# Performance work log

Measured on AMD Instinct MI355X. Metric: run time of the kernel, lower is better.

The kernel has to match this reference:

```python
import jax, jax.numpy as jnp
import numpy as np

TOP_K = 2
N_EXPERTS = 8

def setup_inputs() -> dict:
    key = jax.random.key(0)
    k1, k2, k3, k4 = jax.random.split(key, 4)
    B, C, L, O, E = 8, 4096, 1024, 1024, N_EXPERTS
    scale = 1.0 / np.sqrt(L)
    return {
        "x": jax.random.normal(k1, (B, C, L), dtype=jnp.float32),
        "gate_w": jax.random.normal(k2, (E, L), dtype=jnp.float32) * scale,
        "expert_w": jax.random.normal(k3, (E, O, L), dtype=jnp.float32) * scale,
        "expert_b": jax.random.normal(k4, (E, O), dtype=jnp.float32) * scale,
    }

def reference(x, gate_w, expert_w, expert_b):
    B, C, L = x.shape
    E, O, _ = expert_w.shape
    xt = x.reshape(-1, L)                                  # [T, L], T = B*C
    router_logits = jnp.einsum('tl,el->te', xt, gate_w)    # [T, E]
    probs = jax.nn.softmax(router_logits.astype(jnp.float32), axis=-1)
    routing_weights, selected = jax.lax.top_k(probs, TOP_K)  # [T, K] each
    # combine weight per (token, expert): sum of top-k weights routed to that expert
    comb = jnp.sum(jax.nn.one_hot(selected, E, dtype=routing_weights.dtype)
                   * routing_weights[..., None], axis=1)   # [T, E]
    comb = comb.astype(x.dtype)
    out = jnp.zeros((xt.shape[0], O), dtype=x.dtype)
    for e in range(E):  # small fixed expert loop; masked dense combine
        ye = xt @ expert_w[e].T + expert_b[e]              # [T, O]
        out = out + ye * comb[:, e:e + 1]
    return out.reshape(B, C, O)
```

## Files before the change

### kernel.cpp

```cpp
#include <hip/hip_runtime.h>
#include <cstdint>
#include <cstddef>

#define E_EXP 8
#define LDIM 1024
#define ODIM 1024
#define NPAIR 64

#define BM 256
#define BN 128
#define BK 32
#define NKT (LDIM / BK)
#define MAXRT 160
#define GEMM_GRID (MAXRT * 8)
#define CPX (GEMM_GRID / 8)

typedef __bf16 bf16x8 __attribute__((ext_vector_type(8)));
typedef float f32x4 __attribute__((ext_vector_type(4)));

__device__ __forceinline__ unsigned short f2bf(float f) {
  uint32_t u = __float_as_uint(f);
  u += 0x7FFFu + ((u >> 16) & 1u);
  return (unsigned short)(u >> 16);
}

__device__ __forceinline__ void gload_lds16(const void* g, void* l) {
  __builtin_amdgcn_global_load_lds(
      (const __attribute__((address_space(1))) unsigned int*)g,
      (__attribute__((address_space(3))) unsigned int*)l, 16, 0, 0);
}

__global__ __launch_bounds__(256) void route_kernel(
    const float* __restrict__ x, const float* __restrict__ gate,
    unsigned short* __restrict__ xb, int* __restrict__ sel,
    float2* __restrict__ pw, int T)
{
  const int wid = threadIdx.x >> 6, lane = threadIdx.x & 63;
  const int tok = blockIdx.x * 4 + wid;
  if (tok >= T) return;
  const float* xr = x + (size_t)tok * LDIM;
  unsigned short* xbr = xb + (size_t)tok * LDIM;

  float acc[E_EXP];
#pragma unroll
  for (int e = 0; e < E_EXP; ++e) acc[e] = 0.f;

#pragma unroll
  for (int it = 0; it < 4; ++it) {
    const int c = it * 256 + lane * 4;
    float4 xv = *(const float4*)(xr + c);
    ushort4 bvv;
    bvv.x = f2bf(xv.x); bvv.y = f2bf(xv.y); bvv.z = f2bf(xv.z); bvv.w = f2bf(xv.w);
    *(ushort4*)(xbr + c) = bvv;
#pragma unroll
    for (int e = 0; e < E_EXP; ++e) {
      float4 gv = *(const float4*)(gate + e * LDIM + c);
      acc[e] += xv.x * gv.x + xv.y * gv.y + xv.z * gv.z + xv.w * gv.w;
    }
  }
#pragma unroll
  for (int off = 32; off >= 1; off >>= 1) {
#pragma unroll
    for (int e = 0; e < E_EXP; ++e) acc[e] += __shfl_xor(acc[e], off, 64);
  }
  if (lane == 0) {
    int i1 = 0; float m1 = acc[0];
#pragma unroll
    for (int e = 1; e < E_EXP; ++e) if (acc[e] > m1) { m1 = acc[e]; i1 = e; }
    int i2 = -1; float m2 = -1e30f;
#pragma unroll
    for (int e = 0; e < E_EXP; ++e) if (e != i1 && acc[e] > m2) { m2 = acc[e]; i2 = e; }
    float s = 0.f;
#pragma unroll
    for (int e = 0; e < E_EXP; ++e) s += __expf(acc[e] - m1);
    const float inv = 1.f / s;
    sel[tok] = i1 | (i2 << 4);
    pw[tok] = make_float2(inv, __expf(m2 - m1) * inv);
  }
}

__global__ __launch_bounds__(256) void hist_kernel(
    const int* __restrict__ sel, int* __restrict__ hist2d, int T)
{
  __shared__ int h[NPAIR];
  const int tid = threadIdx.x;
  if (tid < NPAIR) h[tid] = 0;
  __syncthreads();
  const int t0 = blockIdx.x * 2048;
#pragma unroll
  for (int i = 0; i < 8; ++i) {
    const int t = t0 + i * 256 + tid;
    if (t < T) {
      const int s = sel[t];
      const int i1 = s & 15, i2 = (s >> 4) & 15;
      const int lo = i1 < i2 ? i1 : i2, hi = i1 < i2 ? i2 : i1;
      atomicAdd(&h[lo * 8 + hi], 1);
    }
  }
  __syncthreads();
  if (tid < NPAIR) hist2d[blockIdx.x * NPAIR + tid] = h[tid];
}

__global__ void finalize_kernel(
    const int* __restrict__ hist2d, int nb,
    int* __restrict__ blockBase, int4* __restrict__ desc, int* __restrict__ meta)
{
  __shared__ int pcnt[NPAIR], pbase[NPAIR];
  const int p = threadIdx.x;
  if (p < NPAIR) {
    int c = 0;
#pragma unroll 4
    for (int b = 0; b < nb; ++b) c += hist2d[b * NPAIR + p];
    pcnt[p] = c;
  }
  __syncthreads();
  if (p == 0) {
    int s = 0;
    for (int q = 0; q < NPAIR; ++q) { pbase[q] = s; s += pcnt[q]; }
  }
  __syncthreads();
  if (p < NPAIR) {
    int run = pbase[p];
    for (int b = 0; b < nb; ++b) {
      blockBase[b * NPAIR + p] = run;
      run += hist2d[b * NPAIR + p];
    }
  }
  if (p == 0) {
    int rt = 0;
    for (int q = 0; q < NPAIR; ++q) {
      const int lo = q >> 3, hi = q & 7;
      for (int j = 0; j * BM < pcnt[q]; ++j) {
        int rows = pcnt[q] - j * BM; if (rows > BM) rows = BM;
        desc[rt] = make_int4(lo | (hi << 8), pbase[q] + j * BM, rows, 0);
        ++rt;
      }
    }
    meta[0] = rt;
  }
}

__global__ __launch_bounds__(256) void scatter_kernel(
    const int* __restrict__ sel, const float2* __restrict__ pw,
    const int* __restrict__ blockBase, int* __restrict__ tokC,
    float2* __restrict__ wC, int T)
{
  __shared__ int cur[NPAIR];
  const int tid = threadIdx.x;
  if (tid < NPAIR) cur[tid] = blockBase[blockIdx.x * NPAIR + tid];
  __syncthreads();
  const int t0 = blockIdx.x * 2048;
#pragma unroll
  for (int i = 0; i < 8; ++i) {
    const int t = t0 + i * 256 + tid;
    if (t < T) {
      const int s = sel[t];
      const int i1 = s & 15, i2 = (s >> 4) & 15;
      const float2 w = pw[t];
      const int lo = i1 < i2 ? i1 : i2, hi = i1 < i2 ? i2 : i1;
      const float wlo = i1 < i2 ? w.x : w.y;
      const float whi = i1 < i2 ? w.y : w.x;
      const int pos = atomicAdd(&cur[lo * 8 + hi], 1);
      tokC[pos] = t;
      wC[pos] = make_float2(wlo, whi);
    }
  }
}

__global__ __launch_bounds__(256) void convw_kernel(
    const float* __restrict__ w, unsigned short* __restrict__ wb, int n4)
{
  int i = blockIdx.x * 256 + threadIdx.x;
  if (i >= n4) return;
  float4 v = *(const float4*)(w + (size_t)i * 4);
  ushort4 b;
  b.x = f2bf(v.x); b.y = f2bf(v.y); b.z = f2bf(v.z); b.w = f2bf(v.w);
  *(ushort4*)(wb + (size_t)i * 4) = b;
}

__global__ __launch_bounds__(512, 2) void moe_gemm_pair(
    const unsigned short* __restrict__ xb, const unsigned short* __restrict__ wb,
    const float* __restrict__ bias, const int4* __restrict__ desc,
    const int* __restrict__ meta, const int* __restrict__ tokC,
    const float2* __restrict__ wC, float* __restrict__ out)
{
  __shared__ __align__(16) unsigned short ldsA[3][BM * BK];
  __shared__ __align__(16) unsigned short ldsB[3][2 * BN * BK];
  const int tid = threadIdx.x;
  const int lane = tid & 63, w = tid >> 6;
  const int wm = w >> 2, wn = w & 3;

  const int totalRT = meta[0];
  const int swz = ((int)blockIdx.x & 7) * CPX + ((int)blockIdx.x >> 3);
  if (swz >= totalRT * 8) return;
  const int rt = swz >> 3, colTile = swz & 7;
  const int4 d = desc[rt];
  const int lo = d.x & 255, hi = d.x >> 8;
  const int start = d.y, ce = d.z;
  const int* tokL = tokC + start;
  const float2* wgtL = wC + start;

  const int s = lane & 3;
  const int rA0 = w * 32 + (lane >> 2);
  const int rA1 = rA0 + 16;
  const int gA0 = s ^ ((rA0 >> 1) & 3);
  const int gA1 = s ^ ((rA1 >> 1) & 3);
  const int tA0 = tokL[rA0 < ce ? rA0 : ce - 1];
  const int tA1 = tokL[rA1 < ce ? rA1 : ce - 1];
  const char* aSrc0 = (const char*)(xb + (size_t)tA0 * LDIM) + gA0 * 16;
  const char* aSrc1 = (const char*)(xb + (size_t)tA1 * LDIM) + gA1 * 16;
  const int rB = w * 16 + (lane >> 2);
  const int gB = s ^ ((rB >> 1) & 3);
  const int colB = colTile * BN + rB;
  const char* bSrcLo = (const char*)(wb + ((size_t)lo * ODIM + colB) * LDIM) + gB * 16;
  const char* bSrcHi = (const char*)(wb + ((size_t)hi * ODIM + colB) * LDIM) + gB * 16;

  int offA[8], offB[2];
#pragma unroll
  for (int fr = 0; fr < 8; ++fr) {
    const int r = wm * 128 + fr * 16 + (lane & 15);
    offA[fr] = r * BK + (((lane >> 4) ^ ((r >> 1) & 3)) * 8);
  }
#pragma unroll
  for (int fc = 0; fc < 2; ++fc) {
    const int r = wn * 32 + fc * 16 + (lane & 15);
    offB[fc] = r * BK + (((lane >> 4) ^ ((r >> 1) & 3)) * 8);
  }

  auto stage = [&](int b, int kt) {
    const int kb = kt * 64;
    gload_lds16(aSrc0 + kb, &ldsA[b][w * 1024]);
    gload_lds16(aSrc1 + kb, &ldsA[b][w * 1024 + 512]);
    gload_lds16(bSrcLo + kb, &ldsB[b][w * 512]);
    gload_lds16(bSrcHi + kb, &ldsB[b][4096 + w * 512]);
  };

  f32x4 acc[2][8][2] = {};

  stage(0, 0); stage(1, 1);
  asm volatile("s_waitcnt vmcnt(4)" ::: "memory");
  __builtin_amdgcn_s_barrier();

  int buf = 0;
#pragma unroll 1
  for (int kt = 0; kt < NKT; ++kt) {
    const unsigned short* As = &ldsA[buf][0];
    const unsigned short* Bs = &ldsB[buf][0];
    bf16x8 af[8], bl0, bl1, bh0, bh1;
#pragma unroll
    for (int fr = 0; fr < 8; ++fr) af[fr] = *(const bf16x8*)(As + offA[fr]);
    bl0 = *(const bf16x8*)(Bs + offB[0]);
    bl1 = *(const bf16x8*)(Bs + offB[1]);
    bh0 = *(const bf16x8*)(Bs + 4096 + offB[0]);
    bh1 = *(const bf16x8*)(Bs + 4096 + offB[1]);

    int sb = buf + 2; if (sb > 2) sb -= 3;
    stage(sb, kt + 2 < NKT ? kt + 2 : NKT - 1);

    __builtin_amdgcn_s_setprio(1);
#pragma unroll
    for (int fr = 0; fr < 8; ++fr) {
      acc[0][fr][0] = __builtin_amdgcn_mfma_f32_16x16x32_bf16(af[fr], bl0, acc[0][fr][0], 0, 0, 0);
      acc[0][fr][1] = __builtin_amdgcn_mfma_f32_16x16x32_bf16(af[fr], bl1, acc[0][fr][1], 0, 0, 0);
      acc[1][fr][0] = __builtin_amdgcn_mfma_f32_16x16x32_bf16(af[fr], bh0, acc[1][fr][0], 0, 0, 0);
      acc[1][fr][1] = __builtin_amdgcn_mfma_f32_16x16x32_bf16(af[fr], bh1, acc[1][fr][1], 0, 0, 0);
    }
    __builtin_amdgcn_s_setprio(0);

    asm volatile("s_waitcnt lgkmcnt(0)" ::: "memory");
    asm volatile("s_waitcnt vmcnt(4)" ::: "memory");
    __builtin_amdgcn_s_barrier();
    buf = (buf == 2) ? 0 : buf + 1;
  }

  int cols[2]; float bLo[2], bHi[2];
#pragma unroll
  for (int fc = 0; fc < 2; ++fc) {
    cols[fc] = colTile * BN + wn * 32 + fc * 16 + (lane & 15);
    bLo[fc] = bias[lo * ODIM + cols[fc]];
    bHi[fc] = bias[hi * ODIM + cols[fc]];
  }
#pragma unroll
  for (int fr = 0; fr < 8; ++fr) {
#pragma unroll
    for (int rr = 0; rr < 4; ++rr) {
      const int row = wm * 128 + fr * 16 + (lane >> 4) * 4 + rr;
      if (row < ce) {
        const int tok = tokL[row];
        const float2 ww = wgtL[row];
        float* orow = out + (size_t)tok * ODIM;
#pragma unroll
        for (int fc = 0; fc < 2; ++fc)
          orow[cols[fc]] = ww.x * (acc[0][fr][fc][rr] + bLo[fc]) +
                           ww.y * (acc[1][fr][fc][rr] + bHi[fc]);
      }
    }
  }
}

__global__ __launch_bounds__(256) void naive_moe(
    const float* __restrict__ x, const float* __restrict__ gate,
    const float* __restrict__ ew, const float* __restrict__ eb,
    float* __restrict__ out, int T)
{
  const int tok = blockIdx.x, tid = threadIdx.x;
  __shared__ float xs[LDIM];
  __shared__ float logits[E_EXP];
  __shared__ float sw1, sw2; __shared__ int si1, si2;
  for (int i = tid; i < LDIM; i += 256) xs[i] = x[(size_t)tok * LDIM + i];
  __syncthreads();
  const int wid = tid >> 6, lane = tid & 63;
  for (int e = wid; e < E_EXP; e += 4) {
    float a = 0.f;
    for (int i = lane; i < LDIM; i += 64) a += xs[i] * gate[e * LDIM + i];
    for (int off = 32; off >= 1; off >>= 1) a += __shfl_xor(a, off, 64);
    if (lane == 0) logits[e] = a;
  }
  __syncthreads();
  if (tid == 0) {
    int i1 = 0; float m1 = logits[0];
    for (int e = 1; e < E_EXP; ++e) if (logits[e] > m1) { m1 = logits[e]; i1 = e; }
    int i2 = -1; float m2 = -1e30f;
    for (int e = 0; e < E_EXP; ++e) if (e != i1 && logits[e] > m2) { m2 = logits[e]; i2 = e; }
    float s = 0.f;
    for (int e = 0; e < E_EXP; ++e) s += __expf(logits[e] - m1);
    si1 = i1; si2 = i2; sw1 = 1.f / s; sw2 = __expf(m2 - m1) / s;
  }
  __syncthreads();
  const int i1 = si1, i2 = si2; const float w1 = sw1, w2 = sw2;
  for (int o = tid; o < ODIM; o += 256) {
    float a1 = 0.f, a2 = 0.f;
    const float* p1 = ew + ((size_t)i1 * ODIM + o) * LDIM;
    const float* p2 = ew + ((size_t)i2 * ODIM + o) * LDIM;
    for (int l = 0; l < LDIM; ++l) { a1 += xs[l] * p1[l]; a2 += xs[l] * p2[l]; }
    out[(size_t)tok * ODIM + o] =
        w1 * (a1 + eb[i1 * ODIM + o]) + w2 * (a2 + eb[i2 * ODIM + o]);
  }
}

extern "C" void kernel_launch(void* const* d_in, const int* in_sizes, int n_in,
                              void* d_out, int out_size, void* d_ws, size_t ws_size,
                              hipStream_t stream) {
  const float* x    = (const float*)d_in[0];
  const float* gate = (const float*)d_in[1];
  const float* ew   = (const float*)d_in[2];
  const float* eb   = (const float*)d_in[3];
  float* out = (float*)d_out;
  const int T = in_sizes[0] / LDIM;
  const int NB = (T + 2047) / 2048;

  const size_t offSel   = 0;
  const size_t offPw    = offSel + (size_t)T * 4;
  const size_t offHist  = offPw + (size_t)T * 8;
  const size_t offBBase = offHist + (size_t)NB * NPAIR * 4;
  const size_t offDesc  = offBBase + (size_t)NB * NPAIR * 4;
  const size_t offMeta  = offDesc + (size_t)MAXRT * 16;
  const size_t offTokC  = offMeta + 256;
  const size_t offWC    = offTokC + (size_t)T * 4;
  const size_t offXb    = offWC + (size_t)T * 8;
  const size_t offWb    = offXb + (size_t)T * LDIM * 2;
  const size_t need     = offWb + (size_t)E_EXP * ODIM * LDIM * 2;

  if (ws_size < need) {
    naive_moe<<<T, 256, 0, stream>>>(x, gate, ew, eb, out, T);
    return;
  }

  char* ws = (char*)d_ws;

  route_kernel<<<(T + 3) / 4, 256, 0, stream>>>(
      x, gate, (unsigned short*)(ws + offXb), (int*)(ws + offSel),
      (float2*)(ws + offPw), T);

  const int n4 = E_EXP * ODIM * LDIM / 4;
  convw_kernel<<<(n4 + 255) / 256, 256, 0, stream>>>(ew, (unsigned short*)(ws + offWb), n4);

  hist_kernel<<<NB, 256, 0, stream>>>(
      (const int*)(ws + offSel), (int*)(ws + offHist), T);

  finalize_kernel<<<1, 64, 0, stream>>>(
      (const int*)(ws + offHist), NB, (int*)(ws + offBBase),
      (int4*)(ws + offDesc), (int*)(ws + offMeta));

  scatter_kernel<<<NB, 256, 0, stream>>>(
      (const int*)(ws + offSel), (const float2*)(ws + offPw),
      (const int*)(ws + offBBase), (int*)(ws + offTokC),
      (float2*)(ws + offWC), T);

  moe_gemm_pair<<<GEMM_GRID, 512, 0, stream>>>(
      (const unsigned short*)(ws + offXb), (const unsigned short*)(ws + offWb),
      eb, (const int4*)(ws + offDesc), (const int*)(ws + offMeta),
      (const int*)(ws + offTokC), (const float2*)(ws + offWC), out);
}
```

Measured before the change: 273.7 us.

## Switch expert GEMM to 32x32x16 MFMA and batch four tokens per routing wave

The grouped expert GEMM now uses 32x32x16 bf16 MFMA tiles in place of 16x16x32. This halves the MFMA instruction count and changes the LDS fragment offsets and the epilogue row mapping to match. Separately, each routing wave now handles four tokens, so every gate-weight load is reused across four tokens and the grid is a quarter the size. The risks are a higher register count for the 16-wide accumulators, and the routing shuffle reduction now covering four times as many values.

```diff
diff --git a/kernel.cpp b/kernel.cpp
--- a/kernel.cpp
+++ b/kernel.cpp
@@ -17,6 +17,7 @@
 
 typedef __bf16 bf16x8 __attribute__((ext_vector_type(8)));
 typedef float f32x4 __attribute__((ext_vector_type(4)));
+typedef float f32x16 __attribute__((ext_vector_type(16)));
 
 __device__ __forceinline__ unsigned short f2bf(float f) {
   uint32_t u = __float_as_uint(f);
@@ -36,46 +37,63 @@
     float2* __restrict__ pw, int T)
 {
   const int wid = threadIdx.x >> 6, lane = threadIdx.x & 63;
-  const int tok = blockIdx.x * 4 + wid;
-  if (tok >= T) return;
-  const float* xr = x + (size_t)tok * LDIM;
-  unsigned short* xbr = xb + (size_t)tok * LDIM;
-
-  float acc[E_EXP];
-#pragma unroll
-  for (int e = 0; e < E_EXP; ++e) acc[e] = 0.f;
+  const int tokBase = blockIdx.x * 16 + wid * 4;
+  if (tokBase >= T) return;
+  const float* xr = x + (size_t)tokBase * LDIM;
+  unsigned short* xbr = xb + (size_t)tokBase * LDIM;
+
+  float acc[4][E_EXP];
+#pragma unroll
+  for (int j = 0; j < 4; ++j)
+#pragma unroll
+    for (int e = 0; e < E_EXP; ++e) acc[j][e] = 0.f;
 
 #pragma unroll
   for (int it = 0; it < 4; ++it) {
     const int c = it * 256 + lane * 4;
-    float4 xv = *(const float4*)(xr + c);
-    ushort4 bvv;
-    bvv.x = f2bf(xv.x); bvv.y = f2bf(xv.y); bvv.z = f2bf(xv.z); bvv.w = f2bf(xv.w);
-    *(ushort4*)(xbr + c) = bvv;
+    float4 xv[4];
+#pragma unroll
+    for (int j = 0; j < 4; ++j) {
+      xv[j] = *(const float4*)(xr + (size_t)j * LDIM + c);
+      ushort4 bv;
+      bv.x = f2bf(xv[j].x); bv.y = f2bf(xv[j].y);
+      bv.z = f2bf(xv[j].z); bv.w = f2bf(xv[j].w);
+      *(ushort4*)(xbr + (size_t)j * LDIM + c) = bv;
+    }
 #pragma unroll
     for (int e = 0; e < E_EXP; ++e) {
       float4 gv = *(const float4*)(gate + e * LDIM + c);
-      acc[e] += xv.x * gv.x + xv.y * gv.y + xv.z * gv.z + xv.w * gv.w;
+#pragma unroll
+      for (int j = 0; j < 4; ++j)
+        acc[j][e] += xv[j].x * gv.x + xv[j].y * gv.y + xv[j].z * gv.z + xv[j].w * gv.w;
     }
   }
 #pragma unroll
   for (int off = 32; off >= 1; off >>= 1) {
 #pragma unroll
-    for (int e = 0; e < E_EXP; ++e) acc[e] += __shfl_xor(acc[e], off, 64);
-  }
-  if (lane == 0) {
-    int i1 = 0; float m1 = acc[0];
-#pragma unroll
-    for (int e = 1; e < E_EXP; ++e) if (acc[e] > m1) { m1 = acc[e]; i1 = e; }
-    int i2 = -1; float m2 = -1e30f;
-#pragma unroll
-    for (int e = 0; e < E_EXP; ++e) if (e != i1 && acc[e] > m2) { m2 = acc[e]; i2 = e; }
-    float s = 0.f;
-#pragma unroll
-    for (int e = 0; e < E_EXP; ++e) s += __expf(acc[e] - m1);
-    const float inv = 1.f / s;
-    sel[tok] = i1 | (i2 << 4);
-    pw[tok] = make_float2(inv, __expf(m2 - m1) * inv);
+    for (int j = 0; j < 4; ++j)
+#pragma unroll
+      for (int e = 0; e < E_EXP; ++e) acc[j][e] += __shfl_xor(acc[j][e], off, 64);
+  }
+  if (lane < 4) {
+    const int tok = tokBase + lane;
+    if (tok < T) {
+      float lg[E_EXP];
+#pragma unroll
+      for (int e = 0; e < E_EXP; ++e) lg[e] = acc[lane][e];
+      int i1 = 0; float m1 = lg[0];
+#pragma unroll
+      for (int e = 1; e < E_EXP; ++e) if (lg[e] > m1) { m1 = lg[e]; i1 = e; }
+      int i2 = -1; float m2 = -1e30f;
+#pragma unroll
+      for (int e = 0; e < E_EXP; ++e) if (e != i1 && lg[e] > m2) { m2 = lg[e]; i2 = e; }
+      float s = 0.f;
+#pragma unroll
+      for (int e = 0; e < E_EXP; ++e) s += __expf(lg[e] - m1);
+      const float inv = 1.f / s;
+      sel[tok] = i1 | (i2 << 4);
+      pw[tok] = make_float2(inv, __expf(m2 - m1) * inv);
+    }
   }
 }
 
@@ -215,16 +233,23 @@
   const char* bSrcLo = (const char*)(wb + ((size_t)lo * ODIM + colB) * LDIM) + gB * 16;
   const char* bSrcHi = (const char*)(wb + ((size_t)hi * ODIM + colB) * LDIM) + gB * 16;
 
-  int offA[8], offB[2];
-#pragma unroll
-  for (int fr = 0; fr < 8; ++fr) {
-    const int r = wm * 128 + fr * 16 + (lane & 15);
-    offA[fr] = r * BK + (((lane >> 4) ^ ((r >> 1) & 3)) * 8);
-  }
-#pragma unroll
-  for (int fc = 0; fc < 2; ++fc) {
-    const int r = wn * 32 + fc * 16 + (lane & 15);
-    offB[fc] = r * BK + (((lane >> 4) ^ ((r >> 1) & 3)) * 8);
+  int offA[4][2], offB[2];
+#pragma unroll
+  for (int fr = 0; fr < 4; ++fr) {
+    const int r = wm * 128 + fr * 32 + (lane & 31);
+#pragma unroll
+    for (int kk = 0; kk < 2; ++kk) {
+      const int g = kk * 2 + (lane >> 5);
+      offA[fr][kk] = r * BK + ((g ^ ((r >> 1) & 3)) * 8);
+    }
+  }
+  {
+    const int r = wn * 32 + (lane & 31);
+#pragma unroll
+    for (int kk = 0; kk < 2; ++kk) {
+      const int g = kk * 2 + (lane >> 5);
+      offB[kk] = r * BK + ((g ^ ((r >> 1) & 3)) * 8);
+    }
   }
 
   auto stage = [&](int b, int kt) {
@@ -235,7 +260,7 @@
     gload_lds16(bSrcHi + kb, &ldsB[b][4096 + w * 512]);
   };
 
-  f32x4 acc[2][8][2] = {};
+  f32x16 acc[2][4] = {};
 
   stage(0, 0); stage(1, 1);
   asm volatile("s_waitcnt vmcnt(4)" ::: "memory");
@@ -246,24 +271,29 @@
   for (int kt = 0; kt < NKT; ++kt) {
     const unsigned short* As = &ldsA[buf][0];
     const unsigned short* Bs = &ldsB[buf][0];
-    bf16x8 af[8], bl0, bl1, bh0, bh1;
-#pragma unroll
-    for (int fr = 0; fr < 8; ++fr) af[fr] = *(const bf16x8*)(As + offA[fr]);
-    bl0 = *(const bf16x8*)(Bs + offB[0]);
-    bl1 = *(const bf16x8*)(Bs + offB[1]);
-    bh0 = *(const bf16x8*)(Bs + 4096 + offB[0]);
-    bh1 = *(const bf16x8*)(Bs + 4096 + offB[1]);
+    bf16x8 af[4][2], blv[2], bhv[2];
+#pragma unroll
+    for (int fr = 0; fr < 4; ++fr) {
+      af[fr][0] = *(const bf16x8*)(As + offA[fr][0]);
+      af[fr][1] = *(const bf16x8*)(As + offA[fr][1]);
+    }
+#pragma unroll
+    for (int kk = 0; kk < 2; ++kk) {
+      blv[kk] = *(const bf16x8*)(Bs + offB[kk]);
+      bhv[kk] = *(const bf16x8*)(Bs + 4096 + offB[kk]);
+    }
 
     int sb = buf + 2; if (sb > 2) sb -= 3;
     stage(sb, kt + 2 < NKT ? kt + 2 : NKT - 1);
 
     __builtin_amdgcn_s_setprio(1);
 #pragma unroll
-    for (int fr = 0; fr < 8; ++fr) {
-      acc[0][fr][0] = __builtin_amdgcn_mfma_f32_16x16x32_bf16(af[fr], bl0, acc[0][fr][0], 0, 0, 0);
-      acc[0][fr][1] = __builtin_amdgcn_mfma_f32_16x16x32_bf16(af[fr], bl1, acc[0][fr][1], 0, 0, 0);
-      acc[1][fr][0] = __builtin_amdgcn_mfma_f32_16x16x32_bf16(af[fr], bh0, acc[1][fr][0], 0, 0, 0);
-      acc[1][fr][1] = __builtin_amdgcn_mfma_f32_16x16x32_bf16(af[fr], bh1, acc[1][fr][1], 0, 0, 0);
+    for (int kk = 0; kk < 2; ++kk) {
+#pragma unroll
+      for (int fr = 0; fr < 4; ++fr) {
+        acc[0][fr] = __builtin_amdgcn_mfma_f32_32x32x16_bf16(af[fr][kk], blv[kk], acc[0][fr], 0, 0, 0);
+        acc[1][fr] = __builtin_amdgcn_mfma_f32_32x32x16_bf16(af[fr][kk], bhv[kk], acc[1][fr], 0, 0, 0);
+      }
     }
     __builtin_amdgcn_s_setprio(0);
 
@@ -273,26 +303,19 @@
     buf = (buf == 2) ? 0 : buf + 1;
   }
 
-  int cols[2]; float bLo[2], bHi[2];
-#pragma unroll
-  for (int fc = 0; fc < 2; ++fc) {
-    cols[fc] = colTile * BN + wn * 32 + fc * 16 + (lane & 15);
-    bLo[fc] = bias[lo * ODIM + cols[fc]];
-    bHi[fc] = bias[hi * ODIM + cols[fc]];
-  }
-#pragma unroll
-  for (int fr = 0; fr < 8; ++fr) {
-#pragma unroll
-    for (int rr = 0; rr < 4; ++rr) {
-      const int row = wm * 128 + fr * 16 + (lane >> 4) * 4 + rr;
+  const int colL = colTile * BN + wn * 32 + (lane & 31);
+  const float bLo = bias[lo * ODIM + colL];
+  const float bHi = bias[hi * ODIM + colL];
+#pragma unroll
+  for (int fr = 0; fr < 4; ++fr) {
+#pragma unroll
+    for (int r16 = 0; r16 < 16; ++r16) {
+      const int row = wm * 128 + fr * 32 + (r16 & 3) + 8 * (r16 >> 2) + 4 * (lane >> 5);
       if (row < ce) {
         const int tok = tokL[row];
         const float2 ww = wgtL[row];
-        float* orow = out + (size_t)tok * ODIM;
-#pragma unroll
-        for (int fc = 0; fc < 2; ++fc)
-          orow[cols[fc]] = ww.x * (acc[0][fr][fc][rr] + bLo[fc]) +
-                           ww.y * (acc[1][fr][fc][rr] + bHi[fc]);
+        out[(size_t)tok * ODIM + colL] =
+            ww.x * (acc[0][fr][r16] + bLo) + ww.y * (acc[1][fr][r16] + bHi);
       }
     }
   }
@@ -368,7 +391,7 @@
 
   char* ws = (char*)d_ws;
 
-  route_kernel<<<(T + 3) / 4, 256, 0, stream>>>(
+  route_kernel<<<(T + 15) / 16, 256, 0, stream>>>(
       x, gate, (unsigned short*)(ws + offXb), (int*)(ws + offSel),
       (float2*)(ws + offPw), T);
 
```

Measured after the change: 304.2 us. +11.2%, slower.
